# Kernel tuning notes

Measured on AMD Instinct MI355X. Metric: run time of the kernel, lower is better.

Reference implementation:

```python
import jax, jax.numpy as jnp
import numpy as np

# Hard-coded wavelet transform matrices from the module (buffers, not learned)
_M1 = np.array([[0.8664, 0.1026, 0.4852, -0.0574],
                [-0.1026, 0.8664, -0.0574, -0.4852],
                [0.4852, 0.0574, -0.8664, 0.1026],
                [0.0574, -0.4852, -0.1026, -0.8664]], dtype=np.float32)
_M2 = np.array([[1.3968, 0.2212, -0.2212, -1.3968],
                [-0.2212, 1.3968, -1.3968, 0.2212],
                [-0.5412, -1.3066, -1.3066, -0.5412],
                [1.3066, -0.5412, -0.5412, 1.3066]], dtype=np.float32)


def setup_inputs() -> dict:
    key = jax.random.key(0)
    x = jax.random.normal(key, (8, 32, 512, 512), dtype=jnp.float32)
    return {"x": x}


def reference(x):
    M1 = jnp.asarray(_M1)
    M2 = jnp.asarray(_M2)
    b, c, h, w = x.shape
    h1, w1 = h // 2, w // 2
    # im2col with 2x2 kernel, stride 2, pad 0 -> [b, c, 4, h1*w1]
    # patch element order is (y, x): (0,0),(0,1),(1,0),(1,1)
    col = x.reshape(b, c, h1, 2, w1, 2).transpose(0, 1, 3, 5, 2, 4)
    col = col.reshape(b, c, 4, h1 * w1)
    # first 4x4 transform (broadcast over b, c)
    x1 = jnp.einsum('ij,bcjl->bcil', M1, col)  # [b, c, 4, h1*w1]
    t = x1.reshape(b, c, 4, h1, w1)
    # roll subbands 1, 2, 3 as in the original (shifts of -1)
    t1 = jnp.roll(t[:, :, 1], -1, axis=2)
    t2 = jnp.roll(t[:, :, 2], -1, axis=3)
    t3 = jnp.roll(t[:, :, 3], (-1, -1), axis=(2, 3))
    x1r = jnp.stack([t[:, :, 0], t1, t2, t3], axis=2).reshape(b, c, 4, h1 * w1)
    # second 4x4 transform
    x2 = jnp.einsum('ij,bcjl->bcil', M2, x1r)  # [b, c, 4, h1*w1]
    # cat([A,B,C,D], dim=1): subband-major channel layout -> [b, 4c, h1, w1]
    out = x2.reshape(b, c, 4, h1, w1).transpose(0, 2, 1, 3, 4).reshape(b, 4 * c, h1, w1)
    return out
```

## Files before the change

kernel.cpp:

```cpp
#include <hip/hip_runtime.h>


#define H  512
#define W  512
#define H1 256
#define W1 256

#define DOT(m0, m1, m2, m3, q, r, s, t) \
    fmaf((m0), (q), fmaf((m1), (r), fmaf((m2), (s), (m3) * (t))))

__global__ __launch_bounds__(256) void nlwt_kernel(const float* __restrict__ x,
                                                   float* __restrict__ out) {
    const int bc  = blockIdx.y;
    const int pid = (blockIdx.x << 8) + threadIdx.x;
    const int i   = pid >> 7;
    const int jp  = pid & 127;
    const int c0  = jp << 2;
    const int j   = jp << 1;

    const int r0 = i << 1;
    const int r2 = (r0 + 2) & (H - 1);
    const int c4 = (c0 + 4) & (W - 1);

    const float* img = x + (size_t)bc * (H * W);
    const float* p0  = img + r0 * W;
    const float* p1  = p0 + W;
    const float* p2  = img + r2 * W;
    const float* p3  = p2 + W;

    const float4 a0 = *(const float4*)(p0 + c0);
    const float2 e0 = *(const float2*)(p0 + c4);
    const float4 a1 = *(const float4*)(p1 + c0);
    const float2 e1 = *(const float2*)(p1 + c4);
    const float4 a2 = *(const float4*)(p2 + c0);
    const float2 e2 = *(const float2*)(p2 + c4);
    const float4 a3 = *(const float4*)(p3 + c0);
    const float2 e3 = *(const float2*)(p3 + c4);

    const float t0 = DOT( 0.8664f,  0.1026f,  0.4852f, -0.0574f, a0.x, a0.y, a1.x, a1.y);
    const float t1 = DOT(-0.1026f,  0.8664f, -0.0574f, -0.4852f, a2.x, a2.y, a3.x, a3.y);
    const float t2 = DOT( 0.4852f,  0.0574f, -0.8664f,  0.1026f, a0.z, a0.w, a1.z, a1.w);
    const float t3 = DOT( 0.0574f, -0.4852f, -0.1026f, -0.8664f, a2.z, a2.w, a3.z, a3.w);

    const float u0 = DOT( 0.8664f,  0.1026f,  0.4852f, -0.0574f, a0.z, a0.w, a1.z, a1.w);
    const float u1 = DOT(-0.1026f,  0.8664f, -0.0574f, -0.4852f, a2.z, a2.w, a3.z, a3.w);
    const float u2 = DOT( 0.4852f,  0.0574f, -0.8664f,  0.1026f, e0.x, e0.y, e1.x, e1.y);
    const float u3 = DOT( 0.0574f, -0.4852f, -0.1026f, -0.8664f, e2.x, e2.y, e3.x, e3.y);

    const int b  = bc >> 5;
    const int ch = bc & 31;
    float* obase = out + ((size_t)(b * 128 + ch) * (H1 * W1)) + i * W1 + j;
    const size_t sstride = (size_t)32 * H1 * W1;

    float2 o;
    o.x = DOT( 1.3968f,  0.2212f, -0.2212f, -1.3968f, t0, t1, t2, t3);
    o.y = DOT( 1.3968f,  0.2212f, -0.2212f, -1.3968f, u0, u1, u2, u3);
    *(float2*)(obase) = o;
    o.x = DOT(-0.2212f,  1.3968f, -1.3968f,  0.2212f, t0, t1, t2, t3);
    o.y = DOT(-0.2212f,  1.3968f, -1.3968f,  0.2212f, u0, u1, u2, u3);
    *(float2*)(obase + sstride) = o;
    o.x = DOT(-0.5412f, -1.3066f, -1.3066f, -0.5412f, t0, t1, t2, t3);
    o.y = DOT(-0.5412f, -1.3066f, -1.3066f, -0.5412f, u0, u1, u2, u3);
    *(float2*)(obase + 2 * sstride) = o;
    o.x = DOT( 1.3066f, -0.5412f, -0.5412f,  1.3066f, t0, t1, t2, t3);
    o.y = DOT( 1.3066f, -0.5412f, -0.5412f,  1.3066f, u0, u1, u2, u3);
    *(float2*)(obase + 3 * sstride) = o;
}

extern "C" void kernel_launch(void* const* d_in, const int* in_sizes, int n_in,
                              void* d_out, int out_size, void* d_ws, size_t ws_size,
                              hipStream_t stream) {
    const float* x = (const float*)d_in[0];
    float* out = (float*)d_out;
    dim3 grid(128, 256);
    nlwt_kernel<<<grid, 256, 0, stream>>>(x, out);
}
```

Before: 420.7 us.

## Process row strips per thread and reuse loaded rows in registers

Each thread now walks down a strip of 16 output rows, carrying the previously loaded input row pair in registers instead of reloading it. This removes the roughly twofold redundant global reads of input rows caused by the vertical roll neighbour. The grid shrinks accordingly, which increases per-thread serial work and register use and reduces the number of blocks available for latency hiding.

```diff
diff --git a/kernel.cpp b/kernel.cpp
--- a/kernel.cpp
+++ b/kernel.cpp
@@ -5,66 +5,68 @@
 #define W  512
 #define H1 256
 #define W1 256
+#define RS 16
 
 #define DOT(m0, m1, m2, m3, q, r, s, t) \
     fmaf((m0), (q), fmaf((m1), (r), fmaf((m2), (s), (m3) * (t))))
 
 __global__ __launch_bounds__(256) void nlwt_kernel(const float* __restrict__ x,
                                                    float* __restrict__ out) {
-    const int bc  = blockIdx.y;
-    const int pid = (blockIdx.x << 8) + threadIdx.x;
-    const int i   = pid >> 7;
-    const int jp  = pid & 127;
-    const int c0  = jp << 2;
-    const int j   = jp << 1;
-
-    const int r0 = i << 1;
-    const int r2 = (r0 + 2) & (H - 1);
-    const int c4 = (c0 + 4) & (W - 1);
+    const int bc    = blockIdx.y;
+    const int strip = (blockIdx.x << 1) + (threadIdx.x >> 7);
+    const int jp    = threadIdx.x & 127;
+    const int c0    = jp << 2;
+    const int c4    = (c0 + 4) & (W - 1);
+    const int j     = jp << 1;
+    const int i0    = strip * RS;
 
     const float* img = x + (size_t)bc * (H * W);
-    const float* p0  = img + r0 * W;
-    const float* p1  = p0 + W;
-    const float* p2  = img + r2 * W;
-    const float* p3  = p2 + W;
-
-    const float4 a0 = *(const float4*)(p0 + c0);
-    const float2 e0 = *(const float2*)(p0 + c4);
-    const float4 a1 = *(const float4*)(p1 + c0);
-    const float2 e1 = *(const float2*)(p1 + c4);
-    const float4 a2 = *(const float4*)(p2 + c0);
-    const float2 e2 = *(const float2*)(p2 + c4);
-    const float4 a3 = *(const float4*)(p3 + c0);
-    const float2 e3 = *(const float2*)(p3 + c4);
-
-    const float t0 = DOT( 0.8664f,  0.1026f,  0.4852f, -0.0574f, a0.x, a0.y, a1.x, a1.y);
-    const float t1 = DOT(-0.1026f,  0.8664f, -0.0574f, -0.4852f, a2.x, a2.y, a3.x, a3.y);
-    const float t2 = DOT( 0.4852f,  0.0574f, -0.8664f,  0.1026f, a0.z, a0.w, a1.z, a1.w);
-    const float t3 = DOT( 0.0574f, -0.4852f, -0.1026f, -0.8664f, a2.z, a2.w, a3.z, a3.w);
-
-    const float u0 = DOT( 0.8664f,  0.1026f,  0.4852f, -0.0574f, a0.z, a0.w, a1.z, a1.w);
-    const float u1 = DOT(-0.1026f,  0.8664f, -0.0574f, -0.4852f, a2.z, a2.w, a3.z, a3.w);
-    const float u2 = DOT( 0.4852f,  0.0574f, -0.8664f,  0.1026f, e0.x, e0.y, e1.x, e1.y);
-    const float u3 = DOT( 0.0574f, -0.4852f, -0.1026f, -0.8664f, e2.x, e2.y, e3.x, e3.y);
-
-    const int b  = bc >> 5;
-    const int ch = bc & 31;
-    float* obase = out + ((size_t)(b * 128 + ch) * (H1 * W1)) + i * W1 + j;
+    const int b = bc >> 5, ch = bc & 31;
+    float* obase = out + ((size_t)(b * 128 + ch) * (H1 * W1)) + (size_t)i0 * W1 + j;
     const size_t sstride = (size_t)32 * H1 * W1;
 
-    float2 o;
-    o.x = DOT( 1.3968f,  0.2212f, -0.2212f, -1.3968f, t0, t1, t2, t3);
-    o.y = DOT( 1.3968f,  0.2212f, -0.2212f, -1.3968f, u0, u1, u2, u3);
-    *(float2*)(obase) = o;
-    o.x = DOT(-0.2212f,  1.3968f, -1.3968f,  0.2212f, t0, t1, t2, t3);
-    o.y = DOT(-0.2212f,  1.3968f, -1.3968f,  0.2212f, u0, u1, u2, u3);
-    *(float2*)(obase + sstride) = o;
-    o.x = DOT(-0.5412f, -1.3066f, -1.3066f, -0.5412f, t0, t1, t2, t3);
-    o.y = DOT(-0.5412f, -1.3066f, -1.3066f, -0.5412f, u0, u1, u2, u3);
-    *(float2*)(obase + 2 * sstride) = o;
-    o.x = DOT( 1.3066f, -0.5412f, -0.5412f,  1.3066f, t0, t1, t2, t3);
-    o.y = DOT( 1.3066f, -0.5412f, -0.5412f,  1.3066f, u0, u1, u2, u3);
-    *(float2*)(obase + 3 * sstride) = o;
+    const float* p = img + (i0 << 1) * W;
+    float4 A  = *(const float4*)(p + c0);
+    float2 Ae = *(const float2*)(p + c4);
+    float4 B  = *(const float4*)(p + W + c0);
+    float2 Be = *(const float2*)(p + W + c4);
+
+#pragma unroll
+    for (int k = 0; k < RS; ++k) {
+        const int i  = i0 + k;
+        const int r2 = ((i << 1) + 2) & (H - 1);
+        const float* q = img + r2 * W;
+        float4 C  = *(const float4*)(q + c0);
+        float2 Ce = *(const float2*)(q + c4);
+        float4 D  = *(const float4*)(q + W + c0);
+        float2 De = *(const float2*)(q + W + c4);
+
+        const float t0 = DOT( 0.8664f,  0.1026f,  0.4852f, -0.0574f, A.x, A.y, B.x, B.y);
+        const float t2 = DOT( 0.4852f,  0.0574f, -0.8664f,  0.1026f, A.z, A.w, B.z, B.w);
+        const float u0 = DOT( 0.8664f,  0.1026f,  0.4852f, -0.0574f, A.z, A.w, B.z, B.w);
+        const float u2 = DOT( 0.4852f,  0.0574f, -0.8664f,  0.1026f, Ae.x, Ae.y, Be.x, Be.y);
+        const float t1 = DOT(-0.1026f,  0.8664f, -0.0574f, -0.4852f, C.x, C.y, D.x, D.y);
+        const float t3 = DOT( 0.0574f, -0.4852f, -0.1026f, -0.8664f, C.z, C.w, D.z, D.w);
+        const float u1 = DOT(-0.1026f,  0.8664f, -0.0574f, -0.4852f, C.z, C.w, D.z, D.w);
+        const float u3 = DOT( 0.0574f, -0.4852f, -0.1026f, -0.8664f, Ce.x, Ce.y, De.x, De.y);
+
+        float* ob = obase + (size_t)k * W1;
+        float2 o;
+        o.x = DOT( 1.3968f,  0.2212f, -0.2212f, -1.3968f, t0, t1, t2, t3);
+        o.y = DOT( 1.3968f,  0.2212f, -0.2212f, -1.3968f, u0, u1, u2, u3);
+        *(float2*)(ob) = o;
+        o.x = DOT(-0.2212f,  1.3968f, -1.3968f,  0.2212f, t0, t1, t2, t3);
+        o.y = DOT(-0.2212f,  1.3968f, -1.3968f,  0.2212f, u0, u1, u2, u3);
+        *(float2*)(ob + sstride) = o;
+        o.x = DOT(-0.5412f, -1.3066f, -1.3066f, -0.5412f, t0, t1, t2, t3);
+        o.y = DOT(-0.5412f, -1.3066f, -1.3066f, -0.5412f, u0, u1, u2, u3);
+        *(float2*)(ob + 2 * sstride) = o;
+        o.x = DOT( 1.3066f, -0.5412f, -0.5412f,  1.3066f, t0, t1, t2, t3);
+        o.y = DOT( 1.3066f, -0.5412f, -0.5412f,  1.3066f, u0, u1, u2, u3);
+        *(float2*)(ob + 3 * sstride) = o;
+
+        A = C; Ae = Ce; B = D; Be = De;
+    }
 }
 
 extern "C" void kernel_launch(void* const* d_in, const int* in_sizes, int n_in,
@@ -72,6 +74,6 @@
                               hipStream_t stream) {
     const float* x = (const float*)d_in[0];
     float* out = (float*)d_out;
-    dim3 grid(128, 256);
+    dim3 grid(8, 256);
     nlwt_kernel<<<grid, 256, 0, stream>>>(x, out);
 }
```

Result: slower. 429.2 us (+2.0%).
